# Optimization experiments

Hardware: AMD Instinct MI355X
Metric: run time of the kernel (lower is better)

## Reference

```python
import jax, jax.numpy as jnp
import numpy as np

N = 20000
E = 640000

def spmm(rows, cols, vals, x):
    # sparse [N,N] @ dense [N,D] via gather + segment-sum scatter
    return jax.ops.segment_sum(vals[:, None] * x[cols], rows, num_segments=N)

def setup_inputs() -> dict:
    key = jax.random.key(0)
    k1, k2, k3, k4, k5, k6 = jax.random.split(key, 6)
    feat = jax.random.normal(k1, (N, 512), dtype=jnp.float32)
    adj_rows = jax.random.randint(k2, (E,), 0, N, dtype=jnp.int32)
    adj_cols = jax.random.randint(k3, (E,), 0, N, dtype=jnp.int32)
    adj_vals = jax.random.uniform(k4, (E,), dtype=jnp.float32)
    # Xavier-uniform scaled weights
    lim1 = float(np.sqrt(6.0 / (512 + 256)))
    lim2 = float(np.sqrt(6.0 / (256 + 64)))
    W1 = jax.random.uniform(k5, (512, 256), minval=-lim1, maxval=lim1, dtype=jnp.float32)
    W2 = jax.random.uniform(k6, (256, 64), minval=-lim2, maxval=lim2, dtype=jnp.float32)
    return {"feat": feat, "adj_rows": adj_rows, "adj_cols": adj_cols,
            "adj_vals": adj_vals, "W1": W1, "W2": W2}

def reference(feat, adj_rows, adj_cols, adj_vals, W1, W2):
    # layer 1: dense GEMM then sparse aggregation (add_act=False, dropout=0)
    x = feat @ W1                      # [N, hid]
    x = spmm(adj_rows, adj_cols, adj_vals, x)
    # layer 2
    x = x @ W2                         # [N, out]
    z = spmm(adj_rows, adj_cols, adj_vals, x)
    # inner-product decoder (dropout=0 in module construction)
    A_rec = jax.nn.sigmoid(z @ z.T)    # [N, N]
    return (z, A_rec)
```

## Files before the change

kernel.cpp:

```cpp
#include <hip/hip_runtime.h>
#include <hip/hip_bf16.h>

#define NN 20000
#define EE 640000


__device__ __forceinline__ float sigf(float x) {
    return __builtin_amdgcn_rcpf(1.0f + __builtin_amdgcn_exp2f(x * -1.442695041f));
}

__global__ void fill_zero_i32(int* __restrict__ p, int n) {
    int i = blockIdx.x * 256 + threadIdx.x;
    if (i < n) p[i] = 0;
}

__global__ void count_rows(const int* __restrict__ rows, int* __restrict__ cnt, int e) {
    int i = blockIdx.x * 256 + threadIdx.x;
    if (i < e) atomicAdd(&cnt[rows[i]], 1);
}

__global__ __launch_bounds__(1024) void scan_counts(const int* __restrict__ cnt,
                                                    int* __restrict__ off,
                                                    int* __restrict__ cursor, int n) {
    __shared__ int part[1024];
    int tid = threadIdx.x;
    const int per = (n + 1023) / 1024;
    int base = tid * per;
    int s = 0;
    for (int i = 0; i < per; ++i) {
        int idx = base + i;
        if (idx < n) s += cnt[idx];
    }
    part[tid] = s;
    __syncthreads();
    for (int d = 1; d < 1024; d <<= 1) {
        int v = (tid >= d) ? part[tid - d] : 0;
        __syncthreads();
        part[tid] += v;
        __syncthreads();
    }
    int run = (tid == 0) ? 0 : part[tid - 1];
    for (int i = 0; i < per; ++i) {
        int idx = base + i;
        if (idx < n) {
            off[idx] = run;
            cursor[idx] = run;
            run += cnt[idx];
        }
    }
    if (tid == 1023) off[n] = part[1023];
}

__global__ void scatter_edges(const int* __restrict__ rows, const int* __restrict__ cols,
                              const float* __restrict__ vals, int* __restrict__ cursor,
                              int* __restrict__ col_s, float* __restrict__ val_s, int e) {
    int i = blockIdx.x * 256 + threadIdx.x;
    if (i < e) {
        int p = atomicAdd(&cursor[rows[i]], 1);
        col_s[p] = cols[i];
        val_s[p] = vals[i];
    }
}

__global__ __launch_bounds__(256) void sgemm64(const float* __restrict__ A,
                                               const float* __restrict__ B,
                                               float* __restrict__ C, int M, int K, int Nc) {
    __shared__ float As[16][65];
    __shared__ float Bs[16][65];
    int tid = threadIdx.x;
    int tm = (tid >> 4) << 2;
    int tn = (tid & 15) << 2;
    int m0 = blockIdx.y * 64;
    int n0 = blockIdx.x * 64;
    float acc[4][4] = {};
    for (int k0 = 0; k0 < K; k0 += 16) {
        for (int i = tid; i < 64 * 16; i += 256) {
            int r = i >> 4, c = i & 15;
            int gr = m0 + r;
            As[c][r] = (gr < M) ? A[(long)gr * K + k0 + c] : 0.0f;
        }
        for (int i = tid; i < 16 * 64; i += 256) {
            int kk = i >> 6, c = i & 63;
            Bs[kk][c] = B[(long)(k0 + kk) * Nc + n0 + c];
        }
        __syncthreads();
        #pragma unroll
        for (int kk = 0; kk < 16; ++kk) {
            float a[4], b[4];
            #pragma unroll
            for (int x = 0; x < 4; ++x) a[x] = As[kk][tm + x];
            #pragma unroll
            for (int y = 0; y < 4; ++y) b[y] = Bs[kk][tn + y];
            #pragma unroll
            for (int x = 0; x < 4; ++x)
                #pragma unroll
                for (int y = 0; y < 4; ++y)
                    acc[x][y] = fmaf(a[x], b[y], acc[x][y]);
        }
        __syncthreads();
    }
    for (int x = 0; x < 4; ++x) {
        int gr = m0 + tm + x;
        if (gr < M) {
            #pragma unroll
            for (int y = 0; y < 4; ++y) C[(long)gr * Nc + n0 + tn + y] = acc[x][y];
        }
    }
}

__global__ __launch_bounds__(256) void spmm_csr64(const int* __restrict__ off,
                                                  const int* __restrict__ col_s,
                                                  const float* __restrict__ val_s,
                                                  const float* __restrict__ X,
                                                  float* __restrict__ Y,
                                                  float* __restrict__ YT, int n) {
    int row = blockIdx.x * 4 + (threadIdx.x >> 6);
    if (row >= n) return;
    int lane = threadIdx.x & 63;
    int e0 = off[row], e1 = off[row + 1];
    float acc = 0.0f;
    for (int e = e0; e < e1; ++e) {
        acc = fmaf(val_s[e], X[(long)col_s[e] * 64 + lane], acc);
    }
    Y[(long)row * 64 + lane] = acc;
    if (YT) YT[(long)lane * n + row] = acc;
}

__global__ __launch_bounds__(256, 4) void decoder_zzT(const float* __restrict__ ZT,
                                                      float* __restrict__ A, int n) {
    __shared__ float Zi[32][128];
    __shared__ float Zj[32][128];
    int tid = threadIdx.x;
    int i0 = blockIdx.y << 7;
    int j0 = blockIdx.x << 7;
    int tm = (tid >> 4) << 3;
    int c0 = (tid & 15) << 2;
    int sc = (tid & 31) << 2;
    int sk = tid >> 5;
    float acc[8][8] = {};
    for (int k0 = 0; k0 < 64; k0 += 32) {
        if (k0) __syncthreads();
        #pragma unroll
        for (int kq = 0; kq < 32; kq += 8) {
            int k = k0 + kq + sk;
            long rb = (long)k * n;
            float4 vi = make_float4(0.f, 0.f, 0.f, 0.f);
            float4 vj = make_float4(0.f, 0.f, 0.f, 0.f);
            if (i0 + sc + 4 <= n) vi = *(const float4*)(ZT + rb + i0 + sc);
            if (j0 + sc + 4 <= n) vj = *(const float4*)(ZT + rb + j0 + sc);
            *(float4*)&Zi[kq + sk][sc] = vi;
            *(float4*)&Zj[kq + sk][sc] = vj;
        }
        __syncthreads();
        #pragma unroll 8
        for (int k = 0; k < 32; ++k) {
            float a[8], b[8];
            *(float4*)&a[0] = *(const float4*)&Zi[k][tm];
            *(float4*)&a[4] = *(const float4*)&Zi[k][tm + 4];
            *(float4*)&b[0] = *(const float4*)&Zj[k][c0];
            *(float4*)&b[4] = *(const float4*)&Zj[k][c0 + 64];
            #pragma unroll
            for (int x = 0; x < 8; ++x)
                #pragma unroll
                for (int y = 0; y < 8; ++y)
                    acc[x][y] = fmaf(a[x], b[y], acc[x][y]);
        }
    }
    #pragma unroll
    for (int x = 0; x < 8; ++x) {
        int gi = i0 + tm + x;
        if (gi >= n) break;
        long rb = (long)gi * n;
        #pragma unroll
        for (int h = 0; h < 2; ++h) {
            int j = j0 + h * 64 + c0;
            if (j + 4 <= n) {
                float4 o;
                o.x = sigf(acc[x][h * 4 + 0]);
                o.y = sigf(acc[x][h * 4 + 1]);
                o.z = sigf(acc[x][h * 4 + 2]);
                o.w = sigf(acc[x][h * 4 + 3]);
                *(float4*)(A + rb + j) = o;
            } else {
                for (int q = 0; q < 4; ++q)
                    if (j + q < n) A[rb + j + q] = sigf(acc[x][h * 4 + q]);
            }
        }
    }
}

extern "C" void kernel_launch(void* const* d_in, const int* in_sizes, int n_in,
                              void* d_out, int out_size, void* d_ws, size_t ws_size,
                              hipStream_t stream) {
    const float* feat     = (const float*)d_in[0];
    const int*   adj_rows = (const int*)d_in[1];
    const int*   adj_cols = (const int*)d_in[2];
    const float* adj_vals = (const float*)d_in[3];
    const float* W1       = (const float*)d_in[4];
    const float* W2       = (const float*)d_in[5];

    float* out  = (float*)d_out;
    float* z    = out;
    float* Arec = out + (long)NN * 64;

    float* W12   = (float*)d_ws;
    float* h     = W12 + 512 * 64;
    float* hz    = h + (long)NN * 64;
    float* val_s = hz + (long)NN * 64;
    int*   col_s = (int*)(val_s + EE);
    int*   cnt   = col_s + EE;
    int*   off   = cnt + NN;
    int*   cursor= off + NN + 1;
    float* zT    = h;

    fill_zero_i32<<<(NN + 255) / 256, 256, 0, stream>>>(cnt, NN);
    count_rows<<<(EE + 255) / 256, 256, 0, stream>>>(adj_rows, cnt, EE);
    scan_counts<<<1, 1024, 0, stream>>>(cnt, off, cursor, NN);
    scatter_edges<<<(EE + 255) / 256, 256, 0, stream>>>(adj_rows, adj_cols, adj_vals,
                                                        cursor, col_s, val_s, EE);

    sgemm64<<<dim3(1, (512 + 63) / 64), 256, 0, stream>>>(W1, W2, W12, 512, 256, 64);
    sgemm64<<<dim3(1, (NN + 63) / 64), 256, 0, stream>>>(feat, W12, h, NN, 512, 64);

    spmm_csr64<<<(NN + 3) / 4, 256, 0, stream>>>(off, col_s, val_s, h, hz, nullptr, NN);
    spmm_csr64<<<(NN + 3) / 4, 256, 0, stream>>>(off, col_s, val_s, hz, z, zT, NN);

    decoder_zzT<<<dim3((NN + 127) / 128, (NN + 127) / 128), 256, 0, stream>>>(zT, Arec, NN);
}
```

Baseline: 2.367 ms.

## Compute decoder Z·Zᵀ with bf16x3 split MFMA instead of fp32 FMA

The second SpMM now writes z as separate bf16 high and low parts in row-major layout instead of an fp32 transpose. The decoder replaces the shared-memory fp32 FMA tile with MFMA 16x16x32 bf16 instructions, using three products (hh, hl, lh) to approximate fp32 accuracy. Operands are loaded straight from global memory into registers, with no LDS staging. The outputs are written as scalar sigmoid stores strided across columns rather than float4 rows, which may hurt store coalescing on what is likely a 1.6 GB write-bound output.

```diff
diff --git a/kernel.cpp b/kernel.cpp
--- a/kernel.cpp
+++ b/kernel.cpp
@@ -4,6 +4,9 @@
 #define NN 20000
 #define EE 640000
 
+
+typedef float f32x4 __attribute__((ext_vector_type(4)));
+typedef short short8 __attribute__((ext_vector_type(8)));
 
 __device__ __forceinline__ float sigf(float x) {
     return __builtin_amdgcn_rcpf(1.0f + __builtin_amdgcn_exp2f(x * -1.442695041f));
@@ -113,7 +116,8 @@
                                                   const float* __restrict__ val_s,
                                                   const float* __restrict__ X,
                                                   float* __restrict__ Y,
-                                                  float* __restrict__ YT, int n) {
+                                                  __hip_bfloat16* __restrict__ ZH,
+                                                  __hip_bfloat16* __restrict__ ZL, int n) {
     int row = blockIdx.x * 4 + (threadIdx.x >> 6);
     if (row >= n) return;
     int lane = threadIdx.x & 63;
@@ -123,67 +127,67 @@
         acc = fmaf(val_s[e], X[(long)col_s[e] * 64 + lane], acc);
     }
     Y[(long)row * 64 + lane] = acc;
-    if (YT) YT[(long)lane * n + row] = acc;
-}
-
-__global__ __launch_bounds__(256, 4) void decoder_zzT(const float* __restrict__ ZT,
-                                                      float* __restrict__ A, int n) {
-    __shared__ float Zi[32][128];
-    __shared__ float Zj[32][128];
+    if (ZH) {
+        __hip_bfloat16 hi = __float2bfloat16(acc);
+        __hip_bfloat16 lo = __float2bfloat16(acc - __bfloat162float(hi));
+        ZH[(long)row * 64 + lane] = hi;
+        ZL[(long)row * 64 + lane] = lo;
+    }
+}
+
+__global__ __launch_bounds__(256, 2) void decoder_mfma(const __hip_bfloat16* __restrict__ ZH,
+                                                       const __hip_bfloat16* __restrict__ ZL,
+                                                       float* __restrict__ A, int n) {
+    const short8* Zh8 = (const short8*)ZH;
+    const short8* Zl8 = (const short8*)ZL;
     int tid = threadIdx.x;
-    int i0 = blockIdx.y << 7;
-    int j0 = blockIdx.x << 7;
-    int tm = (tid >> 4) << 3;
-    int c0 = (tid & 15) << 2;
-    int sc = (tid & 31) << 2;
-    int sk = tid >> 5;
-    float acc[8][8] = {};
-    for (int k0 = 0; k0 < 64; k0 += 32) {
-        if (k0) __syncthreads();
-        #pragma unroll
-        for (int kq = 0; kq < 32; kq += 8) {
-            int k = k0 + kq + sk;
-            long rb = (long)k * n;
-            float4 vi = make_float4(0.f, 0.f, 0.f, 0.f);
-            float4 vj = make_float4(0.f, 0.f, 0.f, 0.f);
-            if (i0 + sc + 4 <= n) vi = *(const float4*)(ZT + rb + i0 + sc);
-            if (j0 + sc + 4 <= n) vj = *(const float4*)(ZT + rb + j0 + sc);
-            *(float4*)&Zi[kq + sk][sc] = vi;
-            *(float4*)&Zj[kq + sk][sc] = vj;
-        }
-        __syncthreads();
-        #pragma unroll 8
-        for (int k = 0; k < 32; ++k) {
-            float a[8], b[8];
-            *(float4*)&a[0] = *(const float4*)&Zi[k][tm];
-            *(float4*)&a[4] = *(const float4*)&Zi[k][tm + 4];
-            *(float4*)&b[0] = *(const float4*)&Zj[k][c0];
-            *(float4*)&b[4] = *(const float4*)&Zj[k][c0 + 64];
-            #pragma unroll
-            for (int x = 0; x < 8; ++x)
+    int lane = tid & 63;
+    int wid = tid >> 6;
+    int wrow = wid >> 1, wcol = wid & 1;
+    int i0 = (blockIdx.y << 7) + (wrow << 6);
+    int j0 = (blockIdx.x << 7) + (wcol << 6);
+    int r16 = lane & 15;
+    int kg = lane >> 4;
+
+    f32x4 acc[4][4] = {};
+
+    #pragma unroll
+    for (int kc = 0; kc < 2; ++kc) {
+        short8 ah[4], al[4], bh[4], bl[4];
+        #pragma unroll
+        for (int t = 0; t < 4; ++t) {
+            int ra = i0 + t * 16 + r16; ra = (ra < n) ? ra : (n - 1);
+            int rb = j0 + t * 16 + r16; rb = (rb < n) ? rb : (n - 1);
+            long oa = (long)ra * 8 + kc * 4 + kg;
+            long ob = (long)rb * 8 + kc * 4 + kg;
+            ah[t] = Zh8[oa];
+            al[t] = Zl8[oa];
+            bh[t] = Zh8[ob];
+            bl[t] = Zl8[ob];
+        }
+        #pragma unroll
+        for (int ti = 0; ti < 4; ++ti)
+            #pragma unroll
+            for (int tj = 0; tj < 4; ++tj) {
+                acc[ti][tj] = __builtin_amdgcn_mfma_f32_16x16x32_bf16(ah[ti], bh[tj], acc[ti][tj], 0, 0, 0);
+                acc[ti][tj] = __builtin_amdgcn_mfma_f32_16x16x32_bf16(ah[ti], bl[tj], acc[ti][tj], 0, 0, 0);
+                acc[ti][tj] = __builtin_amdgcn_mfma_f32_16x16x32_bf16(al[ti], bh[tj], acc[ti][tj], 0, 0, 0);
+            }
+    }
+
+    #pragma unroll
+    for (int ti = 0; ti < 4; ++ti) {
+        int gib = i0 + ti * 16 + (kg << 2);
+        #pragma unroll
+        for (int q = 0; q < 4; ++q) {
+            int gi = gib + q;
+            if (gi < n) {
+                long rowb = (long)gi * n;
                 #pragma unroll
-                for (int y = 0; y < 8; ++y)
-                    acc[x][y] = fmaf(a[x], b[y], acc[x][y]);
-        }
-    }
-    #pragma unroll
-    for (int x = 0; x < 8; ++x) {
-        int gi = i0 + tm + x;
-        if (gi >= n) break;
-        long rb = (long)gi * n;
-        #pragma unroll
-        for (int h = 0; h < 2; ++h) {
-            int j = j0 + h * 64 + c0;
-            if (j + 4 <= n) {
-                float4 o;
-                o.x = sigf(acc[x][h * 4 + 0]);
-                o.y = sigf(acc[x][h * 4 + 1]);
-                o.z = sigf(acc[x][h * 4 + 2]);
-                o.w = sigf(acc[x][h * 4 + 3]);
-                *(float4*)(A + rb + j) = o;
-            } else {
-                for (int q = 0; q < 4; ++q)
-                    if (j + q < n) A[rb + j + q] = sigf(acc[x][h * 4 + q]);
+                for (int tj = 0; tj < 4; ++tj) {
+                    int gj = j0 + tj * 16 + r16;
+                    if (gj < n) A[rowb + gj] = sigf(acc[ti][tj][q]);
+                }
             }
         }
     }
@@ -211,7 +215,8 @@
     int*   cnt   = col_s + EE;
     int*   off   = cnt + NN;
     int*   cursor= off + NN + 1;
-    float* zT    = h;
+    __hip_bfloat16* zh = (__hip_bfloat16*)h;
+    __hip_bfloat16* zl = zh + (long)NN * 64;
 
     fill_zero_i32<<<(NN + 255) / 256, 256, 0, stream>>>(cnt, NN);
     count_rows<<<(EE + 255) / 256, 256, 0, stream>>>(adj_rows, cnt, EE);
@@ -222,8 +227,9 @@
     sgemm64<<<dim3(1, (512 + 63) / 64), 256, 0, stream>>>(W1, W2, W12, 512, 256, 64);
     sgemm64<<<dim3(1, (NN + 63) / 64), 256, 0, stream>>>(feat, W12, h, NN, 512, 64);
 
-    spmm_csr64<<<(NN + 3) / 4, 256, 0, stream>>>(off, col_s, val_s, h, hz, nullptr, NN);
-    spmm_csr64<<<(NN + 3) / 4, 256, 0, stream>>>(off, col_s, val_s, hz, z, zT, NN);
-
-    decoder_zzT<<<dim3((NN + 127) / 128, (NN + 127) / 128), 256, 0, stream>>>(zT, Arec, NN);
-}
+    spmm_csr64<<<(NN + 3) / 4, 256, 0, stream>>>(off, col_s, val_s, h, hz,
+                                                 nullptr, nullptr, NN);
+    spmm_csr64<<<(NN + 3) / 4, 256, 0, stream>>>(off, col_s, val_s, hz, z, zh, zl, NN);
+
+    decoder_mfma<<<dim3((NN + 127) / 128, (NN + 127) / 128), 256, 0, stream>>>(zh, zl, Arec, NN);
+}
```

New measurement: 2.095 ms. 11.5% less time.
